# Kernel optimization log

Measured on AMD Instinct MI355X. Metric: run time of the kernel, lower is better.

The kernel has to match this reference:

```python
import jax, jax.numpy as jnp
import numpy as np

EMB = 384
H = 6
D = 64
B = 256
T = 256


def setup_inputs() -> dict:
    key = jax.random.key(0)
    ks = jax.random.split(key, 6)
    s = 1.0 / np.sqrt(EMB)
    return {
        "x": jax.random.normal(ks[0], (B, T, EMB), dtype=jnp.float32),
        "wq": jax.random.normal(ks[1], (H, EMB, D), dtype=jnp.float32) * s,
        "wk": jax.random.normal(ks[2], (H, EMB, D), dtype=jnp.float32) * s,
        "wv": jax.random.normal(ks[3], (H, EMB, D), dtype=jnp.float32) * s,
        "w_proj": jax.random.normal(ks[4], (H * D, EMB), dtype=jnp.float32) * s,
        "b_proj": jax.random.normal(ks[5], (EMB,), dtype=jnp.float32) * 0.01,
    }


def reference(x, wq, wk, wv, w_proj, b_proj):
    # x: [B, T, E]; per-head projections stacked over H (dropout in eval mode)
    q = jnp.einsum("bte,hed->bhtd", x, wq)
    k = jnp.einsum("bte,hed->bhtd", x, wk)
    v = jnp.einsum("bte,hed->bhtd", x, wv)
    scale = q.shape[-1] ** -0.5
    scores = jnp.einsum("bhqd,bhkd->bhqk", q, k) * scale  # [B,H,T,T]
    tq = q.shape[2]
    causal = jnp.tril(jnp.ones((tq, tq), dtype=bool))
    scores = jnp.where(causal, scores, -jnp.inf)
    att = jax.nn.softmax(scores, axis=-1)
    out = jnp.einsum("bhqk,bhkd->bhqd", att, v)  # [B,H,T,D]
    out = out.transpose(0, 2, 1, 3).reshape(x.shape[0], tq, -1)  # concat heads
    return out @ w_proj + b_proj
```

## Files before the change

### kernel.cpp

```cpp
#include <hip/hip_runtime.h>
#include <hip/hip_bf16.h>


#define Bn 256
#define Tn 256
#define En 384
#define Hn 6
#define Dn 64

typedef __bf16 bf16x8 __attribute__((ext_vector_type(8)));
typedef float f32x4 __attribute__((ext_vector_type(4)));
typedef unsigned short u16x8 __attribute__((ext_vector_type(8)));

static __device__ __forceinline__ unsigned short f2bf(float f) {
    unsigned int u = __builtin_bit_cast(unsigned int, f);
    u += 0x7fffu + ((u >> 16) & 1u);
    return (unsigned short)(u >> 16);
}

static __device__ __forceinline__ f32x4 mfma16(bf16x8 a, bf16x8 b, f32x4 c) {
    return __builtin_amdgcn_mfma_f32_16x16x32_bf16(a, b, c, 0, 0, 0);
}

static __device__ __forceinline__ void glds16(const unsigned short* g, unsigned short* l) {
    __builtin_amdgcn_global_load_lds(
        (const __attribute__((address_space(1))) unsigned int*)g,
        (__attribute__((address_space(3))) unsigned int*)l, 16, 0, 0);
}

__global__ __launch_bounds__(256) void prep_xcast_kernel(
    const float* __restrict__ wq, const float* __restrict__ wk,
    const float* __restrict__ wv, const float* __restrict__ wp,
    const float* __restrict__ x,
    unsigned short* __restrict__ wt, unsigned short* __restrict__ wpt,
    unsigned short* __restrict__ xb) {
    const int bid = blockIdx.x;
    if (bid < 12288) {
        size_t i = ((size_t)bid * 256 + threadIdx.x) * 8;
        float4 f0 = *(const float4*)(x + i);
        float4 f1 = *(const float4*)(x + i + 4);
        u16x8 p;
        p[0] = f2bf(f0.x); p[1] = f2bf(f0.y); p[2] = f2bf(f0.z); p[3] = f2bf(f0.w);
        p[4] = f2bf(f1.x); p[5] = f2bf(f1.y); p[6] = f2bf(f1.z); p[7] = f2bf(f1.w);
        *(u16x8*)(xb + i) = p;
    } else {
        const int NW = 3 * Hn * Dn * En;
        const int NP = En * En;
        int idx = (bid - 12288) * 256 + threadIdx.x;
        if (idx < NW) {
            int e = idx % En;
            int d = (idx / En) % Dn;
            int h = (idx / (En * Dn)) % Hn;
            int t = idx / (En * Dn * Hn);
            const float* src = (t == 0) ? wq : (t == 1) ? wk : wv;
            wt[idx] = f2bf(src[(h * En + e) * Dn + d]);
        } else if (idx < NW + NP) {
            int j = idx - NW;
            int k = j % En;
            int n = j / En;
            wpt[j] = f2bf(wp[k * En + n]);
        }
    }
}

__global__ __launch_bounds__(256) void qkv_gemm(
    const unsigned short* __restrict__ xb, const unsigned short* __restrict__ wt,
    unsigned short* __restrict__ Qo, unsigned short* __restrict__ Ko,
    unsigned short* __restrict__ Vt) {
    __shared__ unsigned short As[2][128][64];
    __shared__ unsigned short Bs[2][192][64];

    const int bid = blockIdx.x;
    const int swz = (bid & 7) * 384 + (bid >> 3);
    const int h = swz % Hn;
    const int m0 = (swz / Hn) * 128;

    const int tid = threadIdx.x;
    const int wave = tid >> 6, lane = tid & 63;
    const int quad = lane >> 4, l16 = lane & 15;
    const int mw = (wave >> 1) * 64, nw = (wave & 1) * 96;

    f32x4 acc[4][6];
#pragma unroll
    for (int i = 0; i < 4; ++i)
#pragma unroll
        for (int j = 0; j < 6; ++j) acc[i][j] = (f32x4){0.f, 0.f, 0.f, 0.f};

    const int lr = lane >> 3;
    const int js = (lane & 7) ^ lr;

    const unsigned short* ga[4];
#pragma unroll
    for (int i = 0; i < 4; ++i)
        ga[i] = xb + (size_t)(m0 + wave * 32 + i * 8 + lr) * En + js * 8;
    const unsigned short* gb[6];
#pragma unroll
    for (int i = 0; i < 6; ++i) {
        int n = wave * 48 + i * 8 + lr;
        gb[i] = wt + (size_t)(((n >> 6) * Hn + h) * Dn + (n & 63)) * En + js * 8;
    }

#define QKV_STAGE(buf, koff)                                              \
    do {                                                                  \
        _Pragma("unroll") for (int i = 0; i < 4; ++i)                     \
            glds16(ga[i] + (koff), &As[buf][wave * 32 + i * 8][0]);       \
        _Pragma("unroll") for (int i = 0; i < 6; ++i)                     \
            glds16(gb[i] + (koff), &Bs[buf][wave * 48 + i * 8][0]);       \
    } while (0)

    QKV_STAGE(0, 0);
    QKV_STAGE(1, 64);

#pragma unroll
    for (int kb = 0; kb < 6; ++kb) {
        if (kb < 5) asm volatile("s_waitcnt vmcnt(10)" ::: "memory");
        else        asm volatile("s_waitcnt vmcnt(0)" ::: "memory");
        __builtin_amdgcn_s_barrier();

        const int cur = kb & 1;
        __builtin_amdgcn_s_setprio(1);
#pragma unroll
        for (int ks = 0; ks < 2; ++ks) {
            bf16x8 a[4], b[6];
            const int ps = ((ks * 4 + quad) ^ (l16 & 7)) * 8;
#pragma unroll
            for (int mi = 0; mi < 4; ++mi)
                a[mi] = *(const bf16x8*)&As[cur][mw + mi * 16 + l16][ps];
#pragma unroll
            for (int ni = 0; ni < 6; ++ni)
                b[ni] = *(const bf16x8*)&Bs[cur][nw + ni * 16 + l16][ps];
#pragma unroll
            for (int mi = 0; mi < 4; ++mi)
#pragma unroll
                for (int ni = 0; ni < 6; ++ni) acc[mi][ni] = mfma16(a[mi], b[ni], acc[mi][ni]);
        }
        __builtin_amdgcn_s_setprio(0);

        if (kb < 4) {
            __builtin_amdgcn_s_barrier();
            QKV_STAGE(cur, (kb + 2) * 64);
        }
    }
#undef QKV_STAGE

    const int b = m0 >> 8, tbase = m0 & 255;
    unsigned short* qkbase[2] = {
        Qo + (size_t)((b * Hn + h) * Tn) * Dn,
        Ko + (size_t)((b * Hn + h) * Tn) * Dn };
    unsigned short* vdst = Vt + (size_t)((b * Hn + h) * Dn) * Tn;
#pragma unroll
    for (int ni = 0; ni < 6; ++ni) {
        const int ng = nw + ni * 16;
        const int tensor = ng >> 6;
        const int d = (ng & 63) + l16;
        if (tensor < 2) {
            unsigned short* dst = qkbase[tensor];
#pragma unroll
            for (int mi = 0; mi < 4; ++mi)
#pragma unroll
                for (int r = 0; r < 4; ++r) {
                    int t = tbase + mw + mi * 16 + quad * 4 + r;
                    dst[t * Dn + d] = f2bf(acc[mi][ni][r]);
                }
        } else {
#pragma unroll
            for (int mi = 0; mi < 4; ++mi) {
                int t0 = tbase + mw + mi * 16 + quad * 4;
                ushort4 pk;
                pk.x = f2bf(acc[mi][ni][0]);
                pk.y = f2bf(acc[mi][ni][1]);
                pk.z = f2bf(acc[mi][ni][2]);
                pk.w = f2bf(acc[mi][ni][3]);
                *(ushort4*)&vdst[d * Tn + t0] = pk;
            }
        }
    }
}

__global__ __launch_bounds__(256) void attn_kernel(
    const unsigned short* __restrict__ Q, const unsigned short* __restrict__ K,
    const unsigned short* __restrict__ Vt, unsigned short* __restrict__ attout) {
    __shared__ unsigned short Kt[256][64];
    __shared__ unsigned short Vl[64][256];
    __shared__ unsigned short P[4][16][72];

    const int h = blockIdx.x, b = blockIdx.y;
    const unsigned short* Qb = Q + (size_t)((b * Hn + h) * Tn) * Dn;
    const unsigned short* Kb = K + (size_t)((b * Hn + h) * Tn) * Dn;
    const unsigned short* Vb = Vt + (size_t)((b * Hn + h) * Dn) * Tn;

    const int tid = threadIdx.x;
    const int wave = tid >> 6, lane = tid & 63;
    const int quad = lane >> 4, l16 = lane & 15;

    const int grp[4] = {wave, 7 - wave, 8 + wave, 15 - wave};

    {
        const unsigned short* kg = Kb + (size_t)(lane >> 3) * Dn + ((lane & 7) ^ (lane >> 3)) * 8;
#pragma unroll
        for (int i = 0; i < 8; ++i) {
            const int c = wave * 8 + i;
            glds16(kg + (size_t)c * 8 * Dn, &Kt[c * 8][0]);
        }
#pragma unroll
        for (int i = 0; i < 8; ++i) {
            const int c = wave * 8 + i;
            const int d = c * 2 + (lane >> 5);
            const int j = (lane & 31) ^ (d & 7);
            glds16(Vb + (size_t)d * Tn + j * 8, &Vl[c * 2][0]);
        }
    }

    bf16x8 aq[4][2];
#pragma unroll
    for (int gi = 0; gi < 4; ++gi) {
        const int q0 = grp[gi] * 16;
#pragma unroll
        for (int ks = 0; ks < 2; ++ks)
            aq[gi][ks] = *(const bf16x8*)&Qb[(q0 + l16) * Dn + ks * 32 + quad * 8];
    }

    __syncthreads();

    const float cexp = 0.125f * 1.44269504f;

#pragma unroll
    for (int gi = 0; gi < 4; ++gi) {
        const int g = grp[gi];
        const int q0 = g * 16;

        f32x4 O[4];
#pragma unroll
        for (int i = 0; i < 4; ++i) O[i] = (f32x4){0.f, 0.f, 0.f, 0.f};
        float rsum[4] = {0.f, 0.f, 0.f, 0.f};

        const int ktmax = g >> 2;
        for (int kt = 0; kt <= ktmax; ++kt) {
            f32x4 S[4];
#pragma unroll
            for (int i = 0; i < 4; ++i) S[i] = (f32x4){0.f, 0.f, 0.f, 0.f};
            __builtin_amdgcn_s_setprio(1);
#pragma unroll
            for (int ks = 0; ks < 2; ++ks)
#pragma unroll
                for (int ni = 0; ni < 4; ++ni) {
                    bf16x8 bk = *(const bf16x8*)
                        &Kt[kt * 64 + ni * 16 + l16][(((ks * 4 + quad) ^ (l16 & 7)) * 8)];
                    S[ni] = mfma16(aq[gi][ks], bk, S[ni]);
                }
            __builtin_amdgcn_s_setprio(0);

#pragma unroll
            for (int ni = 0; ni < 4; ++ni)
#pragma unroll
                for (int r = 0; r < 4; ++r) {
                    int col = kt * 64 + ni * 16 + l16;
                    float p = exp2f(S[ni][r] * cexp);
                    p = (col > q0 + quad * 4 + r) ? 0.f : p;
                    rsum[r] += p;
                    P[wave][quad * 4 + r][ni * 16 + l16] = f2bf(p);
                }

            __builtin_amdgcn_s_setprio(1);
#pragma unroll
            for (int ks = 0; ks < 2; ++ks) {
                bf16x8 ap = *(const bf16x8*)&P[wave][l16][ks * 32 + quad * 8];
#pragma unroll
                for (int ni = 0; ni < 4; ++ni) {
                    bf16x8 bv = *(const bf16x8*)
                        &Vl[ni * 16 + l16][(((kt * 8 + ks * 4 + quad) ^ (l16 & 7)) * 8)];
                    O[ni] = mfma16(ap, bv, O[ni]);
                }
            }
            __builtin_amdgcn_s_setprio(0);
        }

#pragma unroll
        for (int r = 0; r < 4; ++r) {
            float s = rsum[r];
            s += __shfl_xor(s, 1);
            s += __shfl_xor(s, 2);
            s += __shfl_xor(s, 4);
            s += __shfl_xor(s, 8);
            rsum[r] = s;
        }

#pragma unroll
        for (int r = 0; r < 4; ++r) {
            float inv = 1.0f / rsum[r];
#pragma unroll
            for (int ni = 0; ni < 4; ++ni)
                P[wave][quad * 4 + r][ni * 16 + l16] = f2bf(O[ni][r] * inv);
        }
        const int row = lane >> 2;
        const int colc = (lane & 3) * 16;
        unsigned short* dst = attout + (size_t)(b * Tn + q0 + row) * (Hn * Dn) + h * Dn + colc;
        *(uint4*)dst = *(const uint4*)&P[wave][row][colc];
        *(uint4*)(dst + 8) = *(const uint4*)&P[wave][row][colc + 8];
    }
}

__global__ __launch_bounds__(256) void proj_gemm(
    const unsigned short* __restrict__ attout, const unsigned short* __restrict__ wpt,
    const float* __restrict__ bproj, float* __restrict__ out) {
    __shared__ unsigned short As[2][128][64];
    __shared__ unsigned short Bs[2][128][64];

    const int bid = blockIdx.x;
    const int swz = (bid & 7) * 192 + (bid >> 3);
    const int n0 = (swz % 3) * 128;
    const int m0 = (swz / 3) * 128;

    const int tid = threadIdx.x;
    const int wave = tid >> 6, lane = tid & 63;
    const int quad = lane >> 4, l16 = lane & 15;
    const int mw = (wave >> 1) * 64, nw = (wave & 1) * 64;

    f32x4 acc[4][4];
#pragma unroll
    for (int i = 0; i < 4; ++i)
#pragma unroll
        for (int j = 0; j < 4; ++j) acc[i][j] = (f32x4){0.f, 0.f, 0.f, 0.f};

    const int lr = lane >> 3;
    const int js = (lane & 7) ^ lr;

    const unsigned short* ga[4];
    const unsigned short* gb[4];
#pragma unroll
    for (int i = 0; i < 4; ++i) {
        ga[i] = attout + (size_t)(m0 + wave * 32 + i * 8 + lr) * En + js * 8;
        gb[i] = wpt + (size_t)(n0 + wave * 32 + i * 8 + lr) * En + js * 8;
    }

#define PROJ_STAGE(buf, koff)                                             \
    do {                                                                  \
        _Pragma("unroll") for (int i = 0; i < 4; ++i)                     \
            glds16(ga[i] + (koff), &As[buf][wave * 32 + i * 8][0]);       \
        _Pragma("unroll") for (int i = 0; i < 4; ++i)                     \
            glds16(gb[i] + (koff), &Bs[buf][wave * 32 + i * 8][0]);       \
    } while (0)

    PROJ_STAGE(0, 0);
    PROJ_STAGE(1, 64);

#pragma unroll
    for (int kb = 0; kb < 6; ++kb) {
        if (kb < 5) asm volatile("s_waitcnt vmcnt(8)" ::: "memory");
        else        asm volatile("s_waitcnt vmcnt(0)" ::: "memory");
        __builtin_amdgcn_s_barrier();

        const int cur = kb & 1;
        __builtin_amdgcn_s_setprio(1);
#pragma unroll
        for (int ks = 0; ks < 2; ++ks) {
            bf16x8 a[4], bb[4];
            const int ps = ((ks * 4 + quad) ^ (l16 & 7)) * 8;
#pragma unroll
            for (int mi = 0; mi < 4; ++mi)
                a[mi] = *(const bf16x8*)&As[cur][mw + mi * 16 + l16][ps];
#pragma unroll
            for (int ni = 0; ni < 4; ++ni)
                bb[ni] = *(const bf16x8*)&Bs[cur][nw + ni * 16 + l16][ps];
#pragma unroll
            for (int mi = 0; mi < 4; ++mi)
#pragma unroll
                for (int ni = 0; ni < 4; ++ni) acc[mi][ni] = mfma16(a[mi], bb[ni], acc[mi][ni]);
        }
        __builtin_amdgcn_s_setprio(0);

        if (kb < 4) {
            __builtin_amdgcn_s_barrier();
            PROJ_STAGE(cur, (kb + 2) * 64);
        }
    }
#undef PROJ_STAGE

#pragma unroll
    for (int mi = 0; mi < 4; ++mi)
#pragma unroll
        for (int ni = 0; ni < 4; ++ni)
#pragma unroll
            for (int r = 0; r < 4; ++r) {
                int row = m0 + mw + mi * 16 + quad * 4 + r;
                int col = n0 + nw + ni * 16 + l16;
                out[(size_t)row * En + col] = acc[mi][ni][r] + bproj[col];
            }
}

extern "C" void kernel_launch(void* const* d_in, const int* in_sizes, int n_in,
                              void* d_out, int out_size, void* d_ws, size_t ws_size,
                              hipStream_t stream) {
    const float* x  = (const float*)d_in[0];
    const float* wq = (const float*)d_in[1];
    const float* wk = (const float*)d_in[2];
    const float* wv = (const float*)d_in[3];
    const float* wp = (const float*)d_in[4];
    const float* bp = (const float*)d_in[5];
    float* out = (float*)d_out;

    char* ws = (char*)d_ws;
    const size_t WT_OFF  = 0;
    const size_t WPT_OFF = WT_OFF + 884736;
    const size_t Q_OFF   = WPT_OFF + 294912;
    const size_t K_OFF   = Q_OFF + 50331648ull;
    const size_t VT_OFF  = K_OFF + 50331648ull;
    const size_t XB_OFF  = VT_OFF + 50331648ull;

    unsigned short* wt   = (unsigned short*)(ws + WT_OFF);
    unsigned short* wpt  = (unsigned short*)(ws + WPT_OFF);
    unsigned short* Qd   = (unsigned short*)(ws + Q_OFF);
    unsigned short* Kd   = (unsigned short*)(ws + K_OFF);
    unsigned short* Vtd  = (unsigned short*)(ws + VT_OFF);
    unsigned short* xbd  = (unsigned short*)(ws + XB_OFF);
    unsigned short* ao   = xbd;

    prep_xcast_kernel<<<14592, 256, 0, stream>>>(wq, wk, wv, wp, x, wt, wpt, xbd);
    qkv_gemm<<<3072, 256, 0, stream>>>(xbd, wt, Qd, Kd, Vtd);
    attn_kernel<<<dim3(Hn, Bn), 256, 0, stream>>>(Qd, Kd, Vtd, ao);
    proj_gemm<<<1536, 256, 0, stream>>>(ao, wpt, bp, out);
}
```

Baseline: 344.9 us.

## Deepen QKV GEMM pipeline to four stages with 32-wide K tiles

```diff
diff --git a/kernel.cpp b/kernel.cpp
--- a/kernel.cpp
+++ b/kernel.cpp
@@ -67,8 +67,8 @@
     const unsigned short* __restrict__ xb, const unsigned short* __restrict__ wt,
     unsigned short* __restrict__ Qo, unsigned short* __restrict__ Ko,
     unsigned short* __restrict__ Vt) {
-    __shared__ unsigned short As[2][128][64];
-    __shared__ unsigned short Bs[2][192][64];
+    __shared__ unsigned short As[4][128][32];
+    __shared__ unsigned short Bs[4][192][32];
 
     const int bid = blockIdx.x;
     const int swz = (bid & 7) * 384 + (bid >> 3);
@@ -86,60 +86,55 @@
 #pragma unroll
         for (int j = 0; j < 6; ++j) acc[i][j] = (f32x4){0.f, 0.f, 0.f, 0.f};
 
-    const int lr = lane >> 3;
-    const int js = (lane & 7) ^ lr;
-
-    const unsigned short* ga[4];
-#pragma unroll
-    for (int i = 0; i < 4; ++i)
-        ga[i] = xb + (size_t)(m0 + wave * 32 + i * 8 + lr) * En + js * 8;
-    const unsigned short* gb[6];
-#pragma unroll
-    for (int i = 0; i < 6; ++i) {
-        int n = wave * 48 + i * 8 + lr;
+    const int lrow = lane >> 2;
+    const int js = (lane & 3) ^ ((lane >> 3) & 3);
+
+    const unsigned short* ga[2];
+#pragma unroll
+    for (int i = 0; i < 2; ++i)
+        ga[i] = xb + (size_t)(m0 + wave * 32 + i * 16 + lrow) * En + js * 8;
+    const unsigned short* gb[3];
+#pragma unroll
+    for (int i = 0; i < 3; ++i) {
+        int n = wave * 48 + i * 16 + lrow;
         gb[i] = wt + (size_t)(((n >> 6) * Hn + h) * Dn + (n & 63)) * En + js * 8;
     }
 
 #define QKV_STAGE(buf, koff)                                              \
     do {                                                                  \
-        _Pragma("unroll") for (int i = 0; i < 4; ++i)                     \
-            glds16(ga[i] + (koff), &As[buf][wave * 32 + i * 8][0]);       \
-        _Pragma("unroll") for (int i = 0; i < 6; ++i)                     \
-            glds16(gb[i] + (koff), &Bs[buf][wave * 48 + i * 8][0]);       \
+        glds16(ga[0] + (koff), &As[buf][wave * 32][0]);                   \
+        glds16(ga[1] + (koff), &As[buf][wave * 32 + 16][0]);              \
+        glds16(gb[0] + (koff), &Bs[buf][wave * 48][0]);                   \
+        glds16(gb[1] + (koff), &Bs[buf][wave * 48 + 16][0]);              \
+        glds16(gb[2] + (koff), &Bs[buf][wave * 48 + 32][0]);              \
     } while (0)
 
     QKV_STAGE(0, 0);
-    QKV_STAGE(1, 64);
-
-#pragma unroll
-    for (int kb = 0; kb < 6; ++kb) {
-        if (kb < 5) asm volatile("s_waitcnt vmcnt(10)" ::: "memory");
-        else        asm volatile("s_waitcnt vmcnt(0)" ::: "memory");
+    QKV_STAGE(1, 32);
+    QKV_STAGE(2, 64);
+
+    const int ps = (quad ^ ((l16 >> 1) & 3)) * 8;
+
+#pragma unroll
+    for (int kb = 0; kb < 12; ++kb) {
+        if (kb <= 9)       asm volatile("s_waitcnt vmcnt(10)" ::: "memory");
+        else if (kb == 10) asm volatile("s_waitcnt vmcnt(5)" ::: "memory");
+        else               asm volatile("s_waitcnt vmcnt(0)" ::: "memory");
         __builtin_amdgcn_s_barrier();
-
-        const int cur = kb & 1;
-        __builtin_amdgcn_s_setprio(1);
-#pragma unroll
-        for (int ks = 0; ks < 2; ++ks) {
-            bf16x8 a[4], b[6];
-            const int ps = ((ks * 4 + quad) ^ (l16 & 7)) * 8;
-#pragma unroll
-            for (int mi = 0; mi < 4; ++mi)
-                a[mi] = *(const bf16x8*)&As[cur][mw + mi * 16 + l16][ps];
-#pragma unroll
-            for (int ni = 0; ni < 6; ++ni)
-                b[ni] = *(const bf16x8*)&Bs[cur][nw + ni * 16 + l16][ps];
-#pragma unroll
-            for (int mi = 0; mi < 4; ++mi)
-#pragma unroll
-                for (int ni = 0; ni < 6; ++ni) acc[mi][ni] = mfma16(a[mi], b[ni], acc[mi][ni]);
-        }
-        __builtin_amdgcn_s_setprio(0);
-
-        if (kb < 4) {
-            __builtin_amdgcn_s_barrier();
-            QKV_STAGE(cur, (kb + 2) * 64);
-        }
+        if (kb < 9) QKV_STAGE((kb + 3) & 3, (kb + 3) * 32);
+
+        const int cur = kb & 3;
+        bf16x8 a[4], b[6];
+#pragma unroll
+        for (int mi = 0; mi < 4; ++mi)
+            a[mi] = *(const bf16x8*)&As[cur][mw + mi * 16 + l16][ps];
+#pragma unroll
+        for (int ni = 0; ni < 6; ++ni)
+            b[ni] = *(const bf16x8*)&Bs[cur][nw + ni * 16 + l16][ps];
+#pragma unroll
+        for (int mi = 0; mi < 4; ++mi)
+#pragma unroll
+            for (int ni = 0; ni < 6; ++ni) acc[mi][ni] = mfma16(a[mi], b[ni], acc[mi][ni]);
     }
 #undef QKV_STAGE
 
```

Measured after the change: 360.4 us. 1.05x slower.
